# Optimization experiments

Measured on AMD Instinct MI355X. Metric: run time of the kernel, lower is better.

## Reference

```python
import jax, jax.numpy as jnp
import numpy as np

C_IN = 256
K = 4
C_QK = C_IN // K  # 64


def setup_inputs() -> dict:
    key = jax.random.key(0)
    ks = jax.random.split(key, 9)
    B, C, H, W = 4, C_IN, 64, 64
    s = 0.02
    return {
        "x": jax.random.normal(ks[0], (B, C, H, W), dtype=jnp.float32),
        # 1x1 convs stored as dense [out, in] matrices (kernel_size=1)
        "wq": jax.random.normal(ks[1], (C_QK, C), dtype=jnp.float32) * s,
        "bq": jax.random.normal(ks[2], (C_QK,), dtype=jnp.float32) * s,
        "wk": jax.random.normal(ks[3], (C_QK, C), dtype=jnp.float32) * s,
        "bk": jax.random.normal(ks[4], (C_QK,), dtype=jnp.float32) * s,
        "wv": jax.random.normal(ks[5], (C, C), dtype=jnp.float32) * s,
        "bv": jax.random.normal(ks[6], (C,), dtype=jnp.float32) * s,
        "wg": jax.random.normal(ks[7], (C, C), dtype=jnp.float32) * s,
        "bg": jax.random.normal(ks[8], (C,), dtype=jnp.float32) * s,
    }


def reference(x, wq, bq, wk, bk, wv, bv, wg, bg):
    B, C, H, W = x.shape
    N = H * W
    xf = x.reshape(B, C, N)  # [B, C, N]
    # 1x1 conv == per-pixel linear over channels
    q = jnp.einsum("oc,bcn->bon", wq, xf) + bq[None, :, None]  # [B, Cqk, N]
    k = jnp.einsum("oc,bcn->bon", wk, xf) + bk[None, :, None]  # [B, Cqk, N]
    v = jnp.einsum("oc,bcn->bon", wv, xf) + bv[None, :, None]  # [B, C, N]
    # energy[b, n, m] = <q[:, n], k[:, m]>  (n = query pos, m = key pos)
    energy = jnp.einsum("bon,bom->bnm", q, k)  # [B, N, N]
    energy = jax.nn.elu(energy) / N
    # out[b, c, m] = sum_n v[b, c, n] * energy[b, n, m]
    out = jnp.einsum("bcn,bnm->bcm", v, energy).reshape(B, C, H, W)
    out = jnp.einsum("oc,bchw->bohw", wg, out) + bg[None, :, None, None]
    return out
```

## Files before the change

### kernel.cpp

```cpp
#include <hip/hip_runtime.h>

#define B_ 4
#define C_ 256
#define CQK 64
#define N_ 4096
#define SEG 2
#define SEGN (N_ / SEG)
#define NB 128
#define ITERS (SEGN / NB)
#define TS 512

typedef _Float16 f16;
typedef __attribute__((ext_vector_type(8))) _Float16 f16x8;
typedef __attribute__((ext_vector_type(4))) _Float16 f16x4;
typedef __attribute__((ext_vector_type(4))) float f32x4;
typedef __attribute__((ext_vector_type(4))) float float4v;

#define TILE_OFF(l15, quad) ((l15) * 32 + (quad) * 8)

__global__ __launch_bounds__(256) void prep_w(
    const float* __restrict__ wq, const float* __restrict__ wk,
    const float* __restrict__ wv, const float* __restrict__ wg,
    f16* __restrict__ WQt, f16* __restrict__ WKt, f16* __restrict__ WVt,
    f16* __restrict__ WGt) {
  int chunk = blockIdx.x * 256 + threadIdx.x;
  if (chunk >= 20480) return;
  const float* src;
  f16* dst;
  int lo;
  if (chunk < 2048) { src = wq; dst = WQt; lo = chunk * 8; }
  else if (chunk < 4096) { src = wk; dst = WKt; lo = (chunk - 2048) * 8; }
  else if (chunk < 12288) { src = wv; dst = WVt; lo = (chunk - 4096) * 8; }
  else { src = wg; dst = WGt; lo = (chunk - 12288) * 8; }
  int o = lo >> 8, k = lo & 255;
  f16x8 v;
#pragma unroll
  for (int j = 0; j < 8; j++) v[j] = (f16)src[lo + j];
  *(f16x8*)(dst + ((size_t)(o >> 4) * 8 + (k >> 5)) * TS + (o & 15) * 32 + (k & 31)) = v;
}

__global__ __launch_bounds__(512) void proj(
    const float* __restrict__ x, const f16* __restrict__ WQt,
    const f16* __restrict__ WKt, const f16* __restrict__ WVt,
    const float* __restrict__ bq, const float* __restrict__ bk,
    const float* __restrict__ bv, f16* __restrict__ QTt, f16* __restrict__ KTt,
    f16* __restrict__ Vt) {
  __shared__ float xs[64][65];
  __shared__ f16 xt[4 * 8 * TS];
  int n0 = blockIdx.x * 64;
  int b = blockIdx.y;
  int tid = threadIdx.x, lane = tid & 63, w = tid >> 6;
  int l15 = lane & 15, quad = lane >> 4;
  const float* xb = x + (size_t)b * C_ * N_;

  for (int cc = 0; cc < 4; cc++) {
#pragma unroll
    for (int i = 0; i < 8; i++)
      xs[lane][w * 8 + i] = xb[(size_t)(cc * 64 + w * 8 + i) * N_ + n0 + lane];
    __syncthreads();
    {
      int nt = w >> 1;
      f16x8 v;
#pragma unroll
      for (int j = 0; j < 8; j++)
        v[j] = (f16)xs[nt * 16 + l15][32 * (w & 1) + quad * 8 + j];
      *(f16x8*)(xt + (nt * 8 + cc * 2 + (w & 1)) * TS + l15 * 32 + quad * 8) = v;
    }
    __syncthreads();
  }

  f32x4 acc[3][4];
#pragma unroll
  for (int j = 0; j < 3; j++)
#pragma unroll
    for (int nt = 0; nt < 4; nt++) acc[j][nt] = (f32x4){0.f, 0.f, 0.f, 0.f};

#pragma unroll
  for (int kt = 0; kt < 8; kt++) {
    f16x8 xf[4];
#pragma unroll
    for (int nt = 0; nt < 4; nt++)
      xf[nt] = *(const f16x8*)(xt + (nt * 8 + kt) * TS + TILE_OFF(l15, quad));
#pragma unroll
    for (int j = 0; j < 3; j++) {
      int g = w * 3 + j;
      const f16* Wt;
      int ot;
      bool isV = g < 16;
      if (isV) { Wt = WVt; ot = g; }
      else if (g < 20) { Wt = WQt; ot = g - 16; }
      else { Wt = WKt; ot = g - 20; }
      f16x8 wf = *(const f16x8*)(Wt + ((size_t)ot * 8 + kt) * TS + TILE_OFF(l15, quad));
#pragma unroll
      for (int nt = 0; nt < 4; nt++)
        acc[j][nt] = isV
            ? __builtin_amdgcn_mfma_f32_16x16x32_f16(xf[nt], wf, acc[j][nt], 0, 0, 0)
            : __builtin_amdgcn_mfma_f32_16x16x32_f16(wf, xf[nt], acc[j][nt], 0, 0, 0);
    }
  }

  f16* vbout = Vt + (size_t)b * C_ * N_;
#pragma unroll
  for (int j = 0; j < 3; j++) {
    int g = w * 3 + j;
    if (g < 16) {
      float bvv = bv[16 * g + l15];
#pragma unroll
      for (int nt = 0; nt < 4; nt++) {
        f16x4 vals;
#pragma unroll
        for (int r = 0; r < 4; r++) vals[r] = (f16)(acc[j][nt][r] + bvv);
        *(f16x4*)(vbout + ((size_t)g * 128 + (n0 >> 5) + (nt >> 1)) * TS +
                  l15 * 32 + 16 * (nt & 1) + 4 * quad) = vals;
      }
    } else {
      int oq = (g < 20) ? (g - 16) : (g - 20);
      const float* bias = (g < 20) ? bq : bk;
      f16* ob = ((g < 20) ? QTt : KTt) + (size_t)b * N_ * CQK;
#pragma unroll
      for (int nt = 0; nt < 4; nt++) {
        f16x4 vals;
#pragma unroll
        for (int r = 0; r < 4; r++)
          vals[r] = (f16)(acc[j][nt][r] + bias[16 * oq + 4 * quad + r]);
        *(f16x4*)(ob + (((size_t)(n0 >> 4) + nt) * 2 + (oq >> 1)) * TS + l15 * 32 +
                  16 * (oq & 1) + 4 * quad) = vals;
      }
    }
  }
}

__global__ __launch_bounds__(256, 2) void attn(const f16* __restrict__ qt,
                                               const f16* __restrict__ kt,
                                               const f16* __restrict__ v,
                                               const f16* __restrict__ WGt,
                                               f16* __restrict__ part) {
  __shared__ __align__(16) f16 sPt[2][64][128];
  int sb = blockIdx.x;
  int seg = sb >> 2;
  int b = sb & 3;
  int m0 = blockIdx.y * 64;
  int it0 = (((blockIdx.y >> 5) ^ blockIdx.y) & 1) * (ITERS / 2);
  int tid = threadIdx.x, lane = tid & 63, w = tid >> 6;
  int l15 = lane & 15, quad = lane >> 4;
  const f16* qtb = qt + (size_t)b * N_ * CQK;
  const f16* ktb = kt + (size_t)b * N_ * CQK;
  const f16* vb = v + (size_t)b * C_ * N_;

  f32x4 oacc[4][4];
#pragma unroll
  for (int ct = 0; ct < 4; ct++)
#pragma unroll
    for (int mt = 0; mt < 4; mt++) oacc[ct][mt] = (f32x4){0.f, 0.f, 0.f, 0.f};

  f16x8 kf[4][2];
#pragma unroll
  for (int mt = 0; mt < 4; mt++)
#pragma unroll
    for (int ks = 0; ks < 2; ks++)
      kf[mt][ks] = *(const f16x8*)(ktb + ((size_t)((m0 >> 4) + mt) * 2 + ks) * TS +
                                   TILE_OFF(l15, quad));

  f16x8 qf[2][2];
  {
    int nq = seg * SEGN + it0 * NB;
#pragma unroll
    for (int nt = 0; nt < 2; nt++)
#pragma unroll
      for (int ks = 0; ks < 2; ks++)
        qf[nt][ks] = *(const f16x8*)(qtb +
                                     ((size_t)((nq >> 4) + 2 * w + nt) * 2 + ks) * TS +
                                     TILE_OFF(l15, quad));
  }

  {
    char* buf = (char*)sPt[0];
#pragma unroll
    for (int nt = 0; nt < 2; nt++) {
      f32x4 sacc[4];
#pragma unroll
      for (int mt = 0; mt < 4; mt++) sacc[mt] = (f32x4){0.f, 0.f, 0.f, 0.f};
#pragma unroll
      for (int ks = 0; ks < 2; ks++)
#pragma unroll
        for (int mt = 0; mt < 4; mt++)
          sacc[mt] = __builtin_amdgcn_mfma_f32_16x16x32_f16(qf[nt][ks], kf[mt][ks],
                                                            sacc[mt], 0, 0, 0);
#pragma unroll
      for (int mt = 0; mt < 4; mt++) {
        f16x4 p;
#pragma unroll
        for (int r = 0; r < 4; r++) {
          float s = sacc[mt][r];
          p[r] = (f16)(s > 0.0f ? s : (__expf(s) - 1.0f));
        }
        int row = 16 * mt + l15;
        int colb = (64 * w + 32 * nt + 8 * quad) ^ ((row & 7) << 4);
        *(f16x4*)(buf + row * 256 + colb) = p;
      }
    }
  }
  {
    int nq = seg * SEGN + ((it0 + 1) & (ITERS - 1)) * NB;
#pragma unroll
    for (int nt = 0; nt < 2; nt++)
#pragma unroll
      for (int ks = 0; ks < 2; ks++)
        qf[nt][ks] = *(const f16x8*)(qtb +
                                     ((size_t)((nq >> 4) + 2 * w + nt) * 2 + ks) * TS +
                                     TILE_OFF(l15, quad));
  }
  __syncthreads();

  for (int i = 0; i < ITERS; i++) {
    int it = (i + it0) & (ITERS - 1);
    int n0 = seg * SEGN + it * NB;
    char* rbuf = (char*)sPt[i & 1];
    char* wbuf = (char*)sPt[(i + 1) & 1];
    bool hasNext = (i + 1 < ITERS);

    f16x8 vfA[2][4];
#pragma unroll
    for (int ks = 0; ks < 2; ks++)
#pragma unroll
      for (int ct = 0; ct < 4; ct++)
        vfA[ks][ct] = *(const f16x8*)(vb +
                                      ((size_t)(4 * w + ct) * 128 + (n0 >> 5) + ks) * TS +
                                      TILE_OFF(l15, quad));

    f32x4 s0[4], s1[4];
    if (hasNext) {
#pragma unroll
      for (int mt = 0; mt < 4; mt++) s0[mt] = (f32x4){0.f, 0.f, 0.f, 0.f};
#pragma unroll
      for (int ks = 0; ks < 2; ks++)
#pragma unroll
        for (int mt = 0; mt < 4; mt++)
          s0[mt] = __builtin_amdgcn_mfma_f32_16x16x32_f16(qf[0][ks], kf[mt][ks],
                                                          s0[mt], 0, 0, 0);
    }

    f16x8 pa[4];
#pragma unroll
    for (int mt = 0; mt < 4; mt++) {
      int row = 16 * mt + l15;
      pa[mt] = *(const f16x8*)(rbuf + row * 256 + ((quad * 16) ^ ((row & 7) << 4)));
    }
#pragma unroll
    for (int ct = 0; ct < 4; ct++)
#pragma unroll
      for (int mt = 0; mt < 4; mt++)
        oacc[ct][mt] = __builtin_amdgcn_mfma_f32_16x16x32_f16(vfA[0][ct], pa[mt],
                                                              oacc[ct][mt], 0, 0, 0);

    f16x8 vfB[2][4];
#pragma unroll
    for (int ks = 0; ks < 2; ks++)
#pragma unroll
      for (int ct = 0; ct < 4; ct++)
        vfB[ks][ct] = *(const f16x8*)(vb + ((size_t)(4 * w + ct) * 128 + (n0 >> 5) +
                                            2 + ks) * TS +
                                      TILE_OFF(l15, quad));

    if (hasNext) {
#pragma unroll
      for (int mt = 0; mt < 4; mt++) {
        f16x4 p;
#pragma unroll
        for (int r = 0; r < 4; r++) {
          float s = s0[mt][r];
          p[r] = (f16)(s > 0.0f ? s : (__expf(s) - 1.0f));
        }
        int row = 16 * mt + l15;
        int colb = (64 * w + 8 * quad) ^ ((row & 7) << 4);
        *(f16x4*)(wbuf + row * 256 + colb) = p;
      }
    }

#pragma unroll
    for (int mt = 0; mt < 4; mt++) {
      int row = 16 * mt + l15;
      pa[mt] = *(const f16x8*)(rbuf + row * 256 + ((64 + quad * 16) ^ ((row & 7) << 4)));
    }
#pragma unroll
    for (int ct = 0; ct < 4; ct++)
#pragma unroll
      for (int mt = 0; mt < 4; mt++)
        oacc[ct][mt] = __builtin_amdgcn_mfma_f32_16x16x32_f16(vfA[1][ct], pa[mt],
                                                              oacc[ct][mt], 0, 0, 0);

    if (hasNext) {
#pragma unroll
      for (int mt = 0; mt < 4; mt++) s1[mt] = (f32x4){0.f, 0.f, 0.f, 0.f};
#pragma unroll
      for (int ks = 0; ks < 2; ks++)
#pragma unroll
        for (int mt = 0; mt < 4; mt++)
          s1[mt] = __builtin_amdgcn_mfma_f32_16x16x32_f16(qf[1][ks], kf[mt][ks],
                                                          s1[mt], 0, 0, 0);
    }

#pragma unroll
    for (int mt = 0; mt < 4; mt++) {
      int row = 16 * mt + l15;
      pa[mt] = *(const f16x8*)(rbuf + row * 256 + ((128 + quad * 16) ^ ((row & 7) << 4)));
    }
#pragma unroll
    for (int ct = 0; ct < 4; ct++)
#pragma unroll
      for (int mt = 0; mt < 4; mt++)
        oacc[ct][mt] = __builtin_amdgcn_mfma_f32_16x16x32_f16(vfB[0][ct], pa[mt],
                                                              oacc[ct][mt], 0, 0, 0);

    if (hasNext) {
#pragma unroll
      for (int mt = 0; mt < 4; mt++) {
        f16x4 p;
#pragma unroll
        for (int r = 0; r < 4; r++) {
          float s = s1[mt][r];
          p[r] = (f16)(s > 0.0f ? s : (__expf(s) - 1.0f));
        }
        int row = 16 * mt + l15;
        int colb = (64 * w + 32 + 8 * quad) ^ ((row & 7) << 4);
        *(f16x4*)(wbuf + row * 256 + colb) = p;
      }
      if (i + 2 < ITERS) {
        int nq = seg * SEGN + ((i + 2 + it0) & (ITERS - 1)) * NB;
#pragma unroll
        for (int nt = 0; nt < 2; nt++)
#pragma unroll
          for (int ks = 0; ks < 2; ks++)
            qf[nt][ks] = *(const f16x8*)(qtb +
                                         ((size_t)((nq >> 4) + 2 * w + nt) * 2 + ks) * TS +
                                         TILE_OFF(l15, quad));
      }
    }

#pragma unroll
    for (int mt = 0; mt < 4; mt++) {
      int row = 16 * mt + l15;
      pa[mt] = *(const f16x8*)(rbuf + row * 256 + ((192 + quad * 16) ^ ((row & 7) << 4)));
    }
#pragma unroll
    for (int ct = 0; ct < 4; ct++)
#pragma unroll
      for (int mt = 0; mt < 4; mt++)
        oacc[ct][mt] = __builtin_amdgcn_mfma_f32_16x16x32_f16(vfB[1][ct], pa[mt],
                                                              oacc[ct][mt], 0, 0, 0);

    __syncthreads();
  }

  f16* obuf = (f16*)sPt;
#pragma unroll
  for (int ct = 0; ct < 4; ct++) {
#pragma unroll
    for (int mt = 0; mt < 4; mt++) {
      f16x4 vals;
#pragma unroll
      for (int r = 0; r < 4; r++)
        vals[r] = (f16)(oacc[ct][mt][r] * (1.0f / (float)N_));
      *(f16x4*)(obuf + (mt * 8 + 2 * w + (ct >> 1)) * TS + l15 * 32 +
                16 * (ct & 1) + 4 * quad) = vals;
    }
  }
  __syncthreads();
  f32x4 accO[4][4];
#pragma unroll
  for (int ot = 0; ot < 4; ot++)
#pragma unroll
    for (int mt = 0; mt < 4; mt++) accO[ot][mt] = (f32x4){0.f, 0.f, 0.f, 0.f};
#pragma unroll
  for (int kt = 0; kt < 8; kt++) {
    f16x8 bO[4];
#pragma unroll
    for (int mt = 0; mt < 4; mt++)
      bO[mt] = *(const f16x8*)(obuf + (mt * 8 + kt) * TS + TILE_OFF(l15, quad));
#pragma unroll
    for (int ot = 0; ot < 4; ot++) {
      f16x8 af = *(const f16x8*)(WGt + ((size_t)(4 * w + ot) * 8 + kt) * TS +
                                 TILE_OFF(l15, quad));
#pragma unroll
      for (int mt = 0; mt < 4; mt++)
        accO[ot][mt] = __builtin_amdgcn_mfma_f32_16x16x32_f16(af, bO[mt], accO[ot][mt], 0, 0, 0);
    }
  }
  f16* pb = part + ((size_t)(seg * B_ + b) * C_) * N_;
#pragma unroll
  for (int ot = 0; ot < 4; ot++) {
#pragma unroll
    for (int mt = 0; mt < 4; mt++) {
      int m = m0 + 16 * mt + l15;
#pragma unroll
      for (int r = 0; r < 4; r++) {
        int o = 64 * w + 16 * ot + 4 * quad + r;
        pb[(size_t)o * N_ + m] = (f16)accO[ot][mt][r];
      }
    }
  }
}

__global__ __launch_bounds__(256) void combine(const f16* __restrict__ part,
                                               const float* __restrict__ bg,
                                               float* __restrict__ out) {
  size_t i = ((size_t)blockIdx.x * 256 + threadIdx.x) * 8;
  f16x8 p0 = *(const f16x8*)(part + i);
  f16x8 p1 = *(const f16x8*)(part + (size_t)B_ * C_ * N_ + i);
  float bgo = bg[(i >> 12) & 255];
  float4v r0, r1;
#pragma unroll
  for (int j = 0; j < 4; j++) r0[j] = (float)p0[j] + (float)p1[j] + bgo;
#pragma unroll
  for (int j = 0; j < 4; j++) r1[j] = (float)p0[4 + j] + (float)p1[4 + j] + bgo;
  *(float4v*)(out + i) = r0;
  *(float4v*)(out + i + 4) = r1;
}

extern "C" void kernel_launch(void* const* d_in, const int* in_sizes, int n_in,
                              void* d_out, int out_size, void* d_ws, size_t ws_size,
                              hipStream_t stream) {
  const float* x = (const float*)d_in[0];
  const float* wq = (const float*)d_in[1];
  const float* bq = (const float*)d_in[2];
  const float* wk = (const float*)d_in[3];
  const float* bk = (const float*)d_in[4];
  const float* wv = (const float*)d_in[5];
  const float* bv = (const float*)d_in[6];
  const float* wg = (const float*)d_in[7];
  const float* bg = (const float*)d_in[8];
  float* out = (float*)d_out;

  char* ws = (char*)d_ws;
  f16* QTt = (f16*)ws; ws += (size_t)B_ * N_ * CQK * sizeof(f16);
  f16* KTt = (f16*)ws; ws += (size_t)B_ * N_ * CQK * sizeof(f16);
  f16* Vt  = (f16*)ws; ws += (size_t)B_ * C_ * N_ * sizeof(f16);
  f16* WQt = (f16*)ws; ws += (size_t)CQK * C_ * sizeof(f16);
  f16* WKt = (f16*)ws; ws += (size_t)CQK * C_ * sizeof(f16);
  f16* WVt = (f16*)ws; ws += (size_t)C_ * C_ * sizeof(f16);
  f16* WGt = (f16*)ws; ws += (size_t)C_ * C_ * sizeof(f16);
  f16* PART = (f16*)ws; ws += (size_t)SEG * B_ * C_ * N_ * sizeof(f16);

  prep_w<<<dim3(80), 256, 0, stream>>>(wq, wk, wv, wg, WQt, WKt, WVt, WGt);
  proj<<<dim3(N_ / 64, B_), 512, 0, stream>>>(x, WQt, WKt, WVt, bq, bk, bv,
                                              QTt, KTt, Vt);
  attn<<<dim3(SEG * B_, N_ / 64), 256, 0, stream>>>(QTt, KTt, Vt, WGt, PART);
  combine<<<dim3(2048), 256, 0, stream>>>(PART, bg, out);
}
```

Baseline: 156.9 us.

## Drop split-N partials and combine kernel; tile M by 32 over full N

Removes the two-way split of the attention reduction over N, so partial outputs are no longer written in f16 and summed by a separate combine kernel. Each block now covers 32 output columns over the full N range, applies the gamma projection and bias, and writes the final fp32 output directly. This removes the partial-buffer write and read and one kernel launch. In exchange, each block streams all of V for half as many columns, which halves V reuse per MFMA and doubles total V and Q traffic through L2.

```diff
diff --git a/kernel.cpp b/kernel.cpp
--- a/kernel.cpp
+++ b/kernel.cpp
@@ -4,10 +4,8 @@
 #define C_ 256
 #define CQK 64
 #define N_ 4096
-#define SEG 2
-#define SEGN (N_ / SEG)
 #define NB 128
-#define ITERS (SEGN / NB)
+#define ITERS (N_ / NB)
 #define TS 512
 
 typedef _Float16 f16;
@@ -134,60 +132,56 @@
                                                const f16* __restrict__ kt,
                                                const f16* __restrict__ v,
                                                const f16* __restrict__ WGt,
-                                               f16* __restrict__ part) {
-  __shared__ __align__(16) f16 sPt[2][64][128];
+                                               const float* __restrict__ bg,
+                                               float* __restrict__ out) {
+  __shared__ __align__(16) f16 sPt[2][32][128];
   int sb = blockIdx.x;
-  int seg = sb >> 2;
   int b = sb & 3;
-  int m0 = blockIdx.y * 64;
-  int it0 = (((blockIdx.y >> 5) ^ blockIdx.y) & 1) * (ITERS / 2);
+  int mh = sb >> 2;
+  int m0 = mh * 2048 + blockIdx.y * 32;
   int tid = threadIdx.x, lane = tid & 63, w = tid >> 6;
   int l15 = lane & 15, quad = lane >> 4;
   const f16* qtb = qt + (size_t)b * N_ * CQK;
   const f16* ktb = kt + (size_t)b * N_ * CQK;
   const f16* vb = v + (size_t)b * C_ * N_;
 
-  f32x4 oacc[4][4];
+  f32x4 oacc[4][2];
 #pragma unroll
   for (int ct = 0; ct < 4; ct++)
 #pragma unroll
-    for (int mt = 0; mt < 4; mt++) oacc[ct][mt] = (f32x4){0.f, 0.f, 0.f, 0.f};
-
-  f16x8 kf[4][2];
-#pragma unroll
-  for (int mt = 0; mt < 4; mt++)
+    for (int mt = 0; mt < 2; mt++) oacc[ct][mt] = (f32x4){0.f, 0.f, 0.f, 0.f};
+
+  f16x8 kf[2][2];
+#pragma unroll
+  for (int mt = 0; mt < 2; mt++)
 #pragma unroll
     for (int ks = 0; ks < 2; ks++)
       kf[mt][ks] = *(const f16x8*)(ktb + ((size_t)((m0 >> 4) + mt) * 2 + ks) * TS +
                                    TILE_OFF(l15, quad));
 
   f16x8 qf[2][2];
-  {
-    int nq = seg * SEGN + it0 * NB;
-#pragma unroll
-    for (int nt = 0; nt < 2; nt++)
-#pragma unroll
-      for (int ks = 0; ks < 2; ks++)
-        qf[nt][ks] = *(const f16x8*)(qtb +
-                                     ((size_t)((nq >> 4) + 2 * w + nt) * 2 + ks) * TS +
-                                     TILE_OFF(l15, quad));
-  }
+#pragma unroll
+  for (int nt = 0; nt < 2; nt++)
+#pragma unroll
+    for (int ks = 0; ks < 2; ks++)
+      qf[nt][ks] = *(const f16x8*)(qtb + ((size_t)(2 * w + nt) * 2 + ks) * TS +
+                                   TILE_OFF(l15, quad));
 
   {
     char* buf = (char*)sPt[0];
 #pragma unroll
     for (int nt = 0; nt < 2; nt++) {
-      f32x4 sacc[4];
-#pragma unroll
-      for (int mt = 0; mt < 4; mt++) sacc[mt] = (f32x4){0.f, 0.f, 0.f, 0.f};
+      f32x4 sacc[2];
+#pragma unroll
+      for (int mt = 0; mt < 2; mt++) sacc[mt] = (f32x4){0.f, 0.f, 0.f, 0.f};
 #pragma unroll
       for (int ks = 0; ks < 2; ks++)
 #pragma unroll
-        for (int mt = 0; mt < 4; mt++)
+        for (int mt = 0; mt < 2; mt++)
           sacc[mt] = __builtin_amdgcn_mfma_f32_16x16x32_f16(qf[nt][ks], kf[mt][ks],
                                                             sacc[mt], 0, 0, 0);
 #pragma unroll
-      for (int mt = 0; mt < 4; mt++) {
+      for (int mt = 0; mt < 2; mt++) {
         f16x4 p;
 #pragma unroll
         for (int r = 0; r < 4; r++) {
@@ -201,7 +195,7 @@
     }
   }
   {
-    int nq = seg * SEGN + ((it0 + 1) & (ITERS - 1)) * NB;
+    int nq = NB;
 #pragma unroll
     for (int nt = 0; nt < 2; nt++)
 #pragma unroll
@@ -213,8 +207,7 @@
   __syncthreads();
 
   for (int i = 0; i < ITERS; i++) {
-    int it = (i + it0) & (ITERS - 1);
-    int n0 = seg * SEGN + it * NB;
+    int n0 = i * NB;
     char* rbuf = (char*)sPt[i & 1];
     char* wbuf = (char*)sPt[(i + 1) & 1];
     bool hasNext = (i + 1 < ITERS);
@@ -228,28 +221,28 @@
                                       ((size_t)(4 * w + ct) * 128 + (n0 >> 5) + ks) * TS +
                                       TILE_OFF(l15, quad));
 
-    f32x4 s0[4], s1[4];
+    f32x4 s0[2], s1[2];
     if (hasNext) {
 #pragma unroll
-      for (int mt = 0; mt < 4; mt++) s0[mt] = (f32x4){0.f, 0.f, 0.f, 0.f};
+      for (int mt = 0; mt < 2; mt++) s0[mt] = (f32x4){0.f, 0.f, 0.f, 0.f};
 #pragma unroll
       for (int ks = 0; ks < 2; ks++)
 #pragma unroll
-        for (int mt = 0; mt < 4; mt++)
+        for (int mt = 0; mt < 2; mt++)
           s0[mt] = __builtin_amdgcn_mfma_f32_16x16x32_f16(qf[0][ks], kf[mt][ks],
                                                           s0[mt], 0, 0, 0);
     }
 
-    f16x8 pa[4];
-#pragma unroll
-    for (int mt = 0; mt < 4; mt++) {
+    f16x8 pa[2];
+#pragma unroll
+    for (int mt = 0; mt < 2; mt++) {
       int row = 16 * mt + l15;
       pa[mt] = *(const f16x8*)(rbuf + row * 256 + ((quad * 16) ^ ((row & 7) << 4)));
     }
 #pragma unroll
     for (int ct = 0; ct < 4; ct++)
 #pragma unroll
-      for (int mt = 0; mt < 4; mt++)
+      for (int mt = 0; mt < 2; mt++)
         oacc[ct][mt] = __builtin_amdgcn_mfma_f32_16x16x32_f16(vfA[0][ct], pa[mt],
                                                               oacc[ct][mt], 0, 0, 0);
 
@@ -264,7 +257,7 @@
 
     if (hasNext) {
 #pragma unroll
-      for (int mt = 0; mt < 4; mt++) {
+      for (int mt = 0; mt < 2; mt++) {
         f16x4 p;
 #pragma unroll
         for (int r = 0; r < 4; r++) {
@@ -278,43 +271,43 @@
     }
 
 #pragma unroll
-    for (int mt = 0; mt < 4; mt++) {
+    for (int mt = 0; mt < 2; mt++) {
       int row = 16 * mt + l15;
       pa[mt] = *(const f16x8*)(rbuf + row * 256 + ((64 + quad * 16) ^ ((row & 7) << 4)));
     }
 #pragma unroll
     for (int ct = 0; ct < 4; ct++)
 #pragma unroll
-      for (int mt = 0; mt < 4; mt++)
+      for (int mt = 0; mt < 2; mt++)
         oacc[ct][mt] = __builtin_amdgcn_mfma_f32_16x16x32_f16(vfA[1][ct], pa[mt],
                                                               oacc[ct][mt], 0, 0, 0);
 
     if (hasNext) {
 #pragma unroll
-      for (int mt = 0; mt < 4; mt++) s1[mt] = (f32x4){0.f, 0.f, 0.f, 0.f};
+      for (int mt = 0; mt < 2; mt++) s1[mt] = (f32x4){0.f, 0.f, 0.f, 0.f};
 #pragma unroll
       for (int ks = 0; ks < 2; ks++)
 #pragma unroll
-        for (int mt = 0; mt < 4; mt++)
+        for (int mt = 0; mt < 2; mt++)
           s1[mt] = __builtin_amdgcn_mfma_f32_16x16x32_f16(qf[1][ks], kf[mt][ks],
                                                           s1[mt], 0, 0, 0);
     }
 
 #pragma unroll
-    for (int mt = 0; mt < 4; mt++) {
+    for (int mt = 0; mt < 2; mt++) {
       int row = 16 * mt + l15;
       pa[mt] = *(const f16x8*)(rbuf + row * 256 + ((128 + quad * 16) ^ ((row & 7) << 4)));
     }
 #pragma unroll
     for (int ct = 0; ct < 4; ct++)
 #pragma unroll
-      for (int mt = 0; mt < 4; mt++)
+      for (int mt = 0; mt < 2; mt++)
         oacc[ct][mt] = __builtin_amdgcn_mfma_f32_16x16x32_f16(vfB[0][ct], pa[mt],
                                                               oacc[ct][mt], 0, 0, 0);
 
     if (hasNext) {
 #pragma unroll
-      for (int mt = 0; mt < 4; mt++) {
+      for (int mt = 0; mt < 2; mt++) {
         f16x4 p;
 #pragma unroll
         for (int r = 0; r < 4; r++) {
@@ -326,7 +319,7 @@
         *(f16x4*)(wbuf + row * 256 + colb) = p;
       }
       if (i + 2 < ITERS) {
-        int nq = seg * SEGN + ((i + 2 + it0) & (ITERS - 1)) * NB;
+        int nq = (i + 2) * NB;
 #pragma unroll
         for (int nt = 0; nt < 2; nt++)
 #pragma unroll
@@ -338,14 +331,14 @@
     }
 
 #pragma unroll
-    for (int mt = 0; mt < 4; mt++) {
+    for (int mt = 0; mt < 2; mt++) {
       int row = 16 * mt + l15;
       pa[mt] = *(const f16x8*)(rbuf + row * 256 + ((192 + quad * 16) ^ ((row & 7) << 4)));
     }
 #pragma unroll
     for (int ct = 0; ct < 4; ct++)
 #pragma unroll
-      for (int mt = 0; mt < 4; mt++)
+      for (int mt = 0; mt < 2; mt++)
         oacc[ct][mt] = __builtin_amdgcn_mfma_f32_16x16x32_f16(vfB[1][ct], pa[mt],
                                                               oacc[ct][mt], 0, 0, 0);
 
@@ -356,7 +349,7 @@
 #pragma unroll
   for (int ct = 0; ct < 4; ct++) {
 #pragma unroll
-    for (int mt = 0; mt < 4; mt++) {
+    for (int mt = 0; mt < 2; mt++) {
       f16x4 vals;
 #pragma unroll
       for (int r = 0; r < 4; r++)
@@ -366,55 +359,41 @@
     }
   }
   __syncthreads();
-  f32x4 accO[4][4];
+  f32x4 accO[4][2];
 #pragma unroll
   for (int ot = 0; ot < 4; ot++)
 #pragma unroll
-    for (int mt = 0; mt < 4; mt++) accO[ot][mt] = (f32x4){0.f, 0.f, 0.f, 0.f};
+    for (int mt = 0; mt < 2; mt++) accO[ot][mt] = (f32x4){0.f, 0.f, 0.f, 0.f};
 #pragma unroll
   for (int kt = 0; kt < 8; kt++) {
-    f16x8 bO[4];
-#pragma unroll
-    for (int mt = 0; mt < 4; mt++)
+    f16x8 bO[2];
+#pragma unroll
+    for (int mt = 0; mt < 2; mt++)
       bO[mt] = *(const f16x8*)(obuf + (mt * 8 + kt) * TS + TILE_OFF(l15, quad));
 #pragma unroll
     for (int ot = 0; ot < 4; ot++) {
       f16x8 af = *(const f16x8*)(WGt + ((size_t)(4 * w + ot) * 8 + kt) * TS +
                                  TILE_OFF(l15, quad));
 #pragma unroll
-      for (int mt = 0; mt < 4; mt++)
-        accO[ot][mt] = __builtin_amdgcn_mfma_f32_16x16x32_f16(af, bO[mt], accO[ot][mt], 0, 0, 0);
-    }
-  }
-  f16* pb = part + ((size_t)(seg * B_ + b) * C_) * N_;
+      for (int mt = 0; mt < 2; mt++)
+        accO[ot][mt] = __builtin_amdgcn_mfma_f32_16x16x32_f16(af, bO[mt], accO[ot][mt],
+                                                              0, 0, 0);
+    }
+  }
+  float* ob = out + (size_t)b * C_ * N_;
 #pragma unroll
   for (int ot = 0; ot < 4; ot++) {
-#pragma unroll
-    for (int mt = 0; mt < 4; mt++) {
+    float4v bgq = *(const float4v*)(bg + 64 * w + 16 * ot + 4 * quad);
+#pragma unroll
+    for (int mt = 0; mt < 2; mt++) {
       int m = m0 + 16 * mt + l15;
 #pragma unroll
       for (int r = 0; r < 4; r++) {
         int o = 64 * w + 16 * ot + 4 * quad + r;
-        pb[(size_t)o * N_ + m] = (f16)accO[ot][mt][r];
-      }
-    }
-  }
-}
-
-__global__ __launch_bounds__(256) void combine(const f16* __restrict__ part,
-                                               const float* __restrict__ bg,
-                                               float* __restrict__ out) {
-  size_t i = ((size_t)blockIdx.x * 256 + threadIdx.x) * 8;
-  f16x8 p0 = *(const f16x8*)(part + i);
-  f16x8 p1 = *(const f16x8*)(part + (size_t)B_ * C_ * N_ + i);
-  float bgo = bg[(i >> 12) & 255];
-  float4v r0, r1;
-#pragma unroll
-  for (int j = 0; j < 4; j++) r0[j] = (float)p0[j] + (float)p1[j] + bgo;
-#pragma unroll
-  for (int j = 0; j < 4; j++) r1[j] = (float)p0[4 + j] + (float)p1[4 + j] + bgo;
-  *(float4v*)(out + i) = r0;
-  *(float4v*)(out + i + 4) = r1;
+        ob[(size_t)o * N_ + m] = accO[ot][mt][r] + bgq[r];
+      }
+    }
+  }
 }
 
 extern "C" void kernel_launch(void* const* d_in, const int* in_sizes, int n_in,
@@ -439,11 +418,9 @@
   f16* WKt = (f16*)ws; ws += (size_t)CQK * C_ * sizeof(f16);
   f16* WVt = (f16*)ws; ws += (size_t)C_ * C_ * sizeof(f16);
   f16* WGt = (f16*)ws; ws += (size_t)C_ * C_ * sizeof(f16);
-  f16* PART = (f16*)ws; ws += (size_t)SEG * B_ * C_ * N_ * sizeof(f16);
 
   prep_w<<<dim3(80), 256, 0, stream>>>(wq, wk, wv, wg, WQt, WKt, WVt, WGt);
   proj<<<dim3(N_ / 64, B_), 512, 0, stream>>>(x, WQt, WKt, WVt, bq, bk, bv,
                                               QTt, KTt, Vt);
-  attn<<<dim3(SEG * B_, N_ / 64), 256, 0, stream>>>(QTt, KTt, Vt, WGt, PART);
-  combine<<<dim3(2048), 256, 0, stream>>>(PART, bg, out);
+  attn<<<dim3(8, N_ / 64), 256, 0, stream>>>(QTt, KTt, Vt, WGt, bg, out);
 }
```

New measurement: 179.9 us. +14.6%, slower.
